# Kernel tuning notes

Measured on AMD Instinct MI355X. Metric: run time of the kernel, lower is better.

## Reference

```python
import jax, jax.numpy as jnp
import numpy as np

D = 128      # hidden_dim
NH = 4       # nhead
FF = 64      # dim_feedforward
P = 16       # patch size
C, H, W = 3, 224, 224
NA = 15      # n_actions
BS = 256
NP = (H // P) * (W // P)      # 196 patches
PD = C * P * P                # 768 patch_dim


def _ln(x, s, b):
    m = jnp.mean(x, -1, keepdims=True)
    v = jnp.mean(jnp.square(x - m), -1, keepdims=True)
    return (x - m) / jnp.sqrt(v + 1e-5) * s + b


def _mha(q, k, v, Wqkv, bqkv, Wo, bo):
    # q,k,v: (L, B, D); Wqkv: (D, 3D) jax-layout; torch MultiheadAttention math
    Wq, Wk, Wv = jnp.split(Wqkv, 3, axis=1)
    bq, bk, bv = jnp.split(bqkv, 3)
    hd = D // NH
    Lq, B, _ = q.shape
    Lk = k.shape[0]
    Q = (q @ Wq + bq).reshape(Lq, B, NH, hd)
    K = (k @ Wk + bk).reshape(Lk, B, NH, hd)
    V = (v @ Wv + bv).reshape(Lk, B, NH, hd)
    scores = jnp.einsum('qbhd,kbhd->bhqk', Q, K) * np.float32(1.0 / np.sqrt(hd))
    attn = jax.nn.softmax(scores, axis=-1)
    out = jnp.einsum('bhqk,kbhd->qbhd', attn, V).reshape(Lq, B, D)
    return out @ Wo + bo


def setup_inputs() -> dict:
    key = jax.random.key(0)
    ks = iter(jax.random.split(key, 64))
    n = lambda shape, sc=0.02: (jax.random.normal(next(ks), shape, jnp.float32) * sc)
    inp = {
        'image': jax.random.normal(next(ks), (BS, C, H, W), jnp.float32),
        'angle': jax.random.normal(next(ks), (BS,), jnp.float32),
        'pos_x': jax.random.normal(next(ks), (BS,), jnp.float32),
        'pos_y': jax.random.normal(next(ks), (BS,), jnp.float32),
        'sk': jax.random.normal(next(ks), (BS, 200), jnp.float32),
        'patch_W': n((PD, D)), 'patch_b': n((D,)),
        'pos_emb': n((NP, 1, D), 1.0),
        'enc_qkv_W': n((D, 3 * D)), 'enc_qkv_b': n((3 * D,)),
        'enc_out_W': n((D, D)), 'enc_out_b': n((D,)),
        'enc_ln1_s': jnp.ones((D,)), 'enc_ln1_b': jnp.zeros((D,)),
        'enc_ff1_W': n((D, FF)), 'enc_ff1_b': n((FF,)),
        'enc_ff2_W': n((FF, D)), 'enc_ff2_b': n((D,)),
        'enc_ln2_s': jnp.ones((D,)), 'enc_ln2_b': jnp.zeros((D,)),
        'dec_sa_qkv_W': n((D, 3 * D)), 'dec_sa_qkv_b': n((3 * D,)),
        'dec_sa_out_W': n((D, D)), 'dec_sa_out_b': n((D,)),
        'dec_ca_qkv_W': n((D, 3 * D)), 'dec_ca_qkv_b': n((3 * D,)),
        'dec_ca_out_W': n((D, D)), 'dec_ca_out_b': n((D,)),
        'dec_ln1_s': jnp.ones((D,)), 'dec_ln1_b': jnp.zeros((D,)),
        'dec_ln2_s': jnp.ones((D,)), 'dec_ln2_b': jnp.zeros((D,)),
        'dec_ln3_s': jnp.ones((D,)), 'dec_ln3_b': jnp.zeros((D,)),
        'dec_ff1_W': n((D, FF)), 'dec_ff1_b': n((FF,)),
        'dec_ff2_W': n((FF, D)), 'dec_ff2_b': n((D,)),
        'dec_norm_s': jnp.ones((D,)), 'dec_norm_b': jnp.zeros((D,)),
        'sk1_W': n((200, 256)), 'sk1_b': n((256,)),
        'sk2_W': n((256, 256)), 'sk2_b': n((256,)),
        'sk3_W': n((256, 100)), 'sk3_b': n((100,)),
        'act_W': n((NA + 103, D)), 'act_b': n((D,)),
        'l1_W': n((D, D)), 'l1_b': n((D,)),
        'l2_W': n((D, 1)), 'l2_b': n((1,)),
    }
    return inp


def reference(image, angle, pos_x, pos_y, sk,
              patch_W, patch_b, pos_emb,
              enc_qkv_W, enc_qkv_b, enc_out_W, enc_out_b,
              enc_ln1_s, enc_ln1_b, enc_ff1_W, enc_ff1_b, enc_ff2_W, enc_ff2_b,
              enc_ln2_s, enc_ln2_b,
              dec_sa_qkv_W, dec_sa_qkv_b, dec_sa_out_W, dec_sa_out_b,
              dec_ca_qkv_W, dec_ca_qkv_b, dec_ca_out_W, dec_ca_out_b,
              dec_ln1_s, dec_ln1_b, dec_ln2_s, dec_ln2_b, dec_ln3_s, dec_ln3_b,
              dec_ff1_W, dec_ff1_b, dec_ff2_W, dec_ff2_b,
              dec_norm_s, dec_norm_b,
              sk1_W, sk1_b, sk2_W, sk2_b, sk3_W, sk3_b,
              act_W, act_b, l1_W, l1_b, l2_W, l2_b):
    b = image.shape[0]
    hh, ww = H // P, W // P
    # rearrange 'b c (h p1) (w p2) -> b (h w) (p1 p2 c)'
    x = image.reshape(b, C, hh, P, ww, P).transpose(0, 2, 4, 3, 5, 1).reshape(b, hh * ww, PD)
    src = (x @ patch_W + patch_b).transpose(1, 0, 2) + pos_emb  # (n, b, D)
    # encoder layer (post-norm, dropout=eval)
    s2 = _mha(src, src, src, enc_qkv_W, enc_qkv_b, enc_out_W, enc_out_b)
    src = _ln(src + s2, enc_ln1_s, enc_ln1_b)
    ff = jax.nn.relu(src @ enc_ff1_W + enc_ff1_b) @ enc_ff2_W + enc_ff2_b
    memory = _ln(src + ff, enc_ln2_s, enc_ln2_b)
    # sketch MLP
    s = jax.nn.relu(sk @ sk1_W + sk1_b)
    s = jax.nn.relu(s @ sk2_W + sk2_b)
    s = s @ sk3_W + sk3_b  # (b, 100)
    pos_ang = jnp.stack([angle, pos_x, pos_y], axis=1)  # (b, 3)
    # batched action encoding (replaces python double loop)
    nA = NA
    eye = jnp.broadcast_to(jnp.eye(nA, dtype=image.dtype)[None], (b, nA, nA))
    feats = jnp.concatenate([
        eye,
        jnp.broadcast_to(pos_ang[:, None, :], (b, nA, 3)),
        jnp.broadcast_to(s[:, None, :], (b, nA, 100)),
    ], axis=-1)  # (b, nA, nA+103)
    tgt = (feats @ act_W + act_b).transpose(1, 0, 2)  # (nA, b, D)
    # decoder layer (post-norm)
    t2 = _mha(tgt, tgt, tgt, dec_sa_qkv_W, dec_sa_qkv_b, dec_sa_out_W, dec_sa_out_b)
    tgt = _ln(tgt + t2, dec_ln1_s, dec_ln1_b)
    t2 = _mha(tgt, memory, memory, dec_ca_qkv_W, dec_ca_qkv_b, dec_ca_out_W, dec_ca_out_b)
    tgt = _ln(tgt + t2, dec_ln2_s, dec_ln2_b)
    ff = jax.nn.relu(tgt @ dec_ff1_W + dec_ff1_b) @ dec_ff2_W + dec_ff2_b
    tgt = _ln(tgt + ff, dec_ln3_s, dec_ln3_b)
    out = _ln(tgt, dec_norm_s, dec_norm_b)  # (nA, b, D)
    out = out.transpose(1, 0, 2)  # (b, nA, D)
    q = jax.nn.relu(out @ l1_W + l1_b) @ l2_W + l2_b  # (b, nA, 1)
    return q[..., 0]  # (b, nA)
```

## Files before the change

### kernel.cpp

```cpp
#include <hip/hip_runtime.h>
#include <math.h>

#define BSZ 256
#define DIM 128
#define NHD 4
#define NPATCH 196
#define NACT 15

typedef float f32x4 __attribute__((ext_vector_type(4)));
typedef __bf16 bf16x8 __attribute__((ext_vector_type(8)));
typedef short short8 __attribute__((ext_vector_type(8)));

__device__ __forceinline__ float wred_sum(float v) {
#pragma unroll
    for (int m = 1; m < 64; m <<= 1) v += __shfl_xor(v, m, 64);
    return v;
}
__device__ __forceinline__ float wred_max(float v) {
#pragma unroll
    for (int m = 1; m < 64; m <<= 1) v = fmaxf(v, __shfl_xor(v, m, 64));
    return v;
}
__device__ __forceinline__ ushort f2bf(float f) {
    unsigned u = __float_as_uint(f);
    return (ushort)((u + 0x7fffu + ((u >> 16) & 1u)) >> 16);
}

__global__ __launch_bounds__(256) void k_wconv(
    const float* __restrict__ pW, const float* __restrict__ qkvW,
    const float* __restrict__ outW, const float* __restrict__ ff1W,
    const float* __restrict__ ff2W, const float* __restrict__ ckvW,
    ushort* __restrict__ o)
{
    int i = blockIdx.x * 256 + threadIdx.x;
    if (i < 98304) {
        int n = i / 768, kp = i % 768;
        int c = kp >> 8, q = kp & 255;
        o[i] = f2bf(pW[(q * 3 + c) * 128 + n]); return;
    }
    i -= 98304;
    if (i < 49152) { int n = i >> 7, k = i & 127; o[98304 + i] = f2bf(qkvW[k * 384 + n]); return; }
    i -= 49152;
    if (i < 16384) { int n = i >> 7, k = i & 127; o[147456 + i] = f2bf(outW[k * 128 + n]); return; }
    i -= 16384;
    if (i < 8192)  { int n = i >> 7, k = i & 127; o[163840 + i] = f2bf(ff1W[k * 64 + n]); return; }
    i -= 8192;
    if (i < 8192)  { int n = i >> 6, k = i & 63;  o[172032 + i] = f2bf(ff2W[k * 128 + n]); return; }
    i -= 8192;
    if (i < 32768) { int n = i >> 7, k = i & 127; o[180224 + i] = f2bf(ckvW[k * 384 + 128 + n]); return; }
}

__global__ __launch_bounds__(512) void k_pg_dec1(
    const float* __restrict__ img, const ushort* __restrict__ Wt,
    const float* __restrict__ pbias, const float* __restrict__ pe,
    float* __restrict__ C, ushort* __restrict__ Cb,
    const float* __restrict__ sk,
    const float* __restrict__ W1, const float* __restrict__ b1,
    const float* __restrict__ W2, const float* __restrict__ b2,
    const float* __restrict__ W3, const float* __restrict__ b3,
    const float* __restrict__ ang, const float* __restrict__ px,
    const float* __restrict__ py,
    const float* __restrict__ actW, const float* __restrict__ actb,
    const float* __restrict__ saW, const float* __restrict__ sab,
    const float* __restrict__ saoW, const float* __restrict__ saob,
    const float* __restrict__ ln1s, const float* __restrict__ ln1b,
    const float* __restrict__ caW, const float* __restrict__ cab,
    float* __restrict__ TGo, float* __restrict__ DQ)
{
    extern __shared__ char smem[];
    const int t = threadIdx.x;
    const int w = t >> 6, l = t & 63;

    if (blockIdx.x >= 256) {
        ushort* As = (ushort*)smem;
        ushort* Ws = As + 2 * 64 * 64;
        const bool act = t < 256;
        const int pb = blockIdx.x - 256;
        const int p = pb >> 2, bq = pb & 3;
        const int hp_ = p / 14, wp = p % 14;
        const int r0 = p * 256 + bq * 64;
        const int wm = w >> 1, wn = w & 1;
        const int lrow = l & 15, lk = l >> 4;
        const int arow = (t & 255) >> 2;
        const int b_img = bq * 64 + arow;
        const float* gimg = img + (size_t)b_img * 150528 + hp_ * 3584 + wp * 16;

        f32x4 acc[2][4];
#pragma unroll
        for (int m = 0; m < 2; ++m)
#pragma unroll
            for (int n = 0; n < 4; ++n) acc[m][n] = (f32x4)0.f;

        float4 va[4];
        short8 wr[4];

        auto loadT = [&](int kc) {
            if (!act) return;
            const int c = kc >> 8, p1q = (kc >> 6) & 3;
            const float* gc = gimg + c * 50176 + p1q * 896;
#pragma unroll
            for (int i = 0; i < 4; ++i)
                va[i] = *(const float4*)(gc + i * 224 + (t & 3) * 4);
#pragma unroll
            for (int j = 0; j < 4; ++j) {
                const int i2 = t + 256 * j;
                const int row = i2 >> 3, ch = i2 & 7;
                wr[j] = *(const short8*)(Wt + (size_t)row * 768 + kc + ch * 8);
            }
        };
        auto storeT = [&](int buf) {
            if (!act) return;
            ushort* Ab = As + buf * 64 * 64;
            ushort* Wb = Ws + buf * 128 * 64;
#pragma unroll
            for (int i = 0; i < 4; ++i) {
                ushort4 o4;
                o4.x = f2bf(va[i].x); o4.y = f2bf(va[i].y);
                o4.z = f2bf(va[i].z); o4.w = f2bf(va[i].w);
                const int kq = (t & 3) + 4 * i;
                const int bo = (kq * 8) ^ ((arow & 7) << 4);
                *(ushort4*)((char*)Ab + arow * 128 + bo) = o4;
            }
#pragma unroll
            for (int j = 0; j < 4; ++j) {
                const int i2 = t + 256 * j;
                const int row = i2 >> 3, ch = i2 & 7;
                const int sw = (ch * 16) ^ ((row & 7) << 4);
                *(short8*)((char*)Wb + row * 128 + sw) = wr[j];
            }
        };
        auto mfmaT = [&](int buf) {
            if (!act) return;
            const ushort* Ab = As + buf * 64 * 64;
            const ushort* Wb = Ws + buf * 128 * 64;
#pragma unroll
            for (int ks = 0; ks < 2; ++ks) {
                bf16x8 af[2], bfr[4];
#pragma unroll
                for (int m = 0; m < 2; ++m) {
                    const int row = wm * 32 + m * 16 + lrow;
                    const int col = (ks * 64 + lk * 16) ^ ((row & 7) << 4);
                    af[m] = *(const bf16x8*)((const char*)Ab + row * 128 + col);
                }
#pragma unroll
                for (int n = 0; n < 4; ++n) {
                    const int row = wn * 64 + n * 16 + lrow;
                    const int col = (ks * 64 + lk * 16) ^ ((row & 7) << 4);
                    bfr[n] = *(const bf16x8*)((const char*)Wb + row * 128 + col);
                }
#pragma unroll
                for (int m = 0; m < 2; ++m)
#pragma unroll
                    for (int n = 0; n < 4; ++n)
                        acc[m][n] = __builtin_amdgcn_mfma_f32_16x16x32_bf16(
                            af[m], bfr[n], acc[m][n], 0, 0, 0);
            }
        };

        loadT(0);
        for (int it = 0; it < 12; it += 2) {
            storeT(0);
            if (it + 1 < 12) loadT((it + 1) * 64);
            __syncthreads();
            mfmaT(0);
            storeT(1);
            if (it + 2 < 12) loadT((it + 2) * 64);
            __syncthreads();
            mfmaT(1);
        }

        if (act) {
            const int crow0 = (l >> 4) * 4;
            const int ccol = l & 15;
#pragma unroll
            for (int m = 0; m < 2; ++m) {
                const int growb = r0 + wm * 32 + m * 16 + crow0;
#pragma unroll
                for (int n = 0; n < 4; ++n) {
                    const int gcol = wn * 64 + n * 16 + ccol;
                    const float bv = pbias[gcol] + pe[p * 128 + gcol];
#pragma unroll
                    for (int j = 0; j < 4; ++j) {
                        const int grow = growb + j;
                        const float v = acc[m][n][j] + bv;
                        C[(size_t)grow * 128 + gcol] = v;
                        Cb[(size_t)grow * 128 + gcol] = f2bf(v);
                    }
                }
            }
        }
        return;
    }

    float* tg  = (float*)smem;
    float* qkv = tg + 1920;
    float* ao  = qkv + 5820;
    float* xr  = ao + 1920;
    float* h1  = xr + 256;
    float* h2  = h1 + 256;
    float* s3  = h2 + 256;
    float* pbv = s3 + 100;
    float* hp  = pbv + 64;
    const int b = blockIdx.x;

    if (t < 256) xr[t] = (t < 200) ? sk[(size_t)b * 200 + t] : 0.f;
    __syncthreads();
    {
        const int c = t & 255, g = t >> 8;
        const int k0 = g * 100;
        float a = 0.f;
#pragma unroll 10
        for (int k = k0; k < k0 + 100; ++k) a += xr[k] * W1[k * 256 + c];
        hp[g * 256 + c] = a;
    }
    __syncthreads();
    if (t < 256) h1[t] = fmaxf(hp[t] + hp[256 + t] + b1[t], 0.f);
    __syncthreads();
    {
        const int c = t & 255, g = t >> 8;
        const int k0 = g * 128;
        float a = 0.f;
#pragma unroll 8
        for (int k = k0; k < k0 + 128; ++k) a += h1[k] * W2[k * 256 + c];
        hp[g * 256 + c] = a;
    }
    __syncthreads();
    if (t < 256) h2[t] = fmaxf(hp[t] + hp[256 + t] + b2[t], 0.f);
    __syncthreads();
    if (t < 400) {
        const int c = t % 100, g = t / 100;
        const int k0 = g * 64;
        float a = 0.f;
#pragma unroll 8
        for (int k = k0; k < k0 + 64; ++k) a += h2[k] * W3[k * 100 + c];
        hp[g * 256 + c] = a;
    }
    __syncthreads();
    if (t < 100) s3[t] = hp[t] + hp[256 + t] + hp[512 + t] + hp[768 + t] + b3[t];
    __syncthreads();
    {
        const int c = t & 127, g = t >> 7;
        const int k0 = g * 25;
        float a = 0.f;
#pragma unroll 5
        for (int k = k0; k < k0 + 25; ++k) a += s3[k] * actW[(18 + k) * 128 + c];
        hp[g * 256 + c] = a;
    }
    __syncthreads();
    if (t < 128) {
        const float base = actb[t] + hp[t] + hp[256 + t] + hp[512 + t] + hp[768 + t] +
                           ang[b] * actW[15 * 128 + t] + px[b] * actW[16 * 128 + t] +
                           py[b] * actW[17 * 128 + t];
#pragma unroll
        for (int i = 0; i < 15; ++i) tg[i * 128 + t] = base + actW[i * 128 + t];
    }
    __syncthreads();

    if (t < 384) {
        float acc[15];
#pragma unroll
        for (int r = 0; r < 15; ++r) acc[r] = 0.f;
#pragma unroll 4
        for (int k = 0; k < 128; ++k) {
            const float wv = saW[(size_t)k * 384 + t];
#pragma unroll
            for (int r = 0; r < 15; ++r) acc[r] += tg[r * 128 + k] * wv;
        }
        const float bb = sab[t];
#pragma unroll
        for (int r = 0; r < 15; ++r) qkv[r * 388 + t] = acc[r] + bb;
    }
    __syncthreads();

    const float rs = 0.17677669529663687f;
    if (w < 4) {
        for (int qi = 0; qi < 15; ++qi) {
            float s = -3.0e38f;
            if (l < 15) {
                s = 0.f;
#pragma unroll
                for (int d = 0; d < 32; ++d)
                    s += qkv[qi * 388 + w * 32 + d] * qkv[l * 388 + 128 + w * 32 + d];
                s *= rs;
            }
            const float m = wred_max(s);
            const float pv = (l < 15) ? __expf(s - m) : 0.f;
            const float sum = wred_sum(pv);
            if (l < 15) pbv[w * 16 + l] = pv;
            if (l < 32) {
                float o = 0.f;
#pragma unroll
                for (int j = 0; j < 15; ++j) o += pbv[w * 16 + j] * qkv[j * 388 + 256 + w * 32 + l];
                ao[qi * 128 + w * 32 + l] = o / sum;
            }
        }
    }
    __syncthreads();

    {
        const int c = t & 127, g = t >> 7;
        const int r3 = (g + 12 < 15) ? g + 12 : 0;
        float a0 = 0.f, a1 = 0.f, a2 = 0.f, a3 = 0.f;
#pragma unroll 4
        for (int k = 0; k < 128; ++k) {
            const float wv = saoW[(size_t)k * 128 + c];
            a0 += ao[g * 128 + k] * wv;
            a1 += ao[(g + 4) * 128 + k] * wv;
            a2 += ao[(g + 8) * 128 + k] * wv;
            a3 += ao[r3 * 128 + k] * wv;
        }
        const float bb = saob[c];
        qkv[g * 388 + c]       = a0 + bb + tg[g * 128 + c];
        qkv[(g + 4) * 388 + c] = a1 + bb + tg[(g + 4) * 128 + c];
        qkv[(g + 8) * 388 + c] = a2 + bb + tg[(g + 8) * 128 + c];
        if (g + 12 < 15) qkv[(g + 12) * 388 + c] = a3 + bb + tg[(g + 12) * 128 + c];
    }
    __syncthreads();
    for (int r = w; r < 15; r += 8) {
        const float x0 = qkv[r * 388 + l], x1 = qkv[r * 388 + l + 64];
        const float sm = wred_sum(x0 + x1);
        const float sq = wred_sum(x0 * x0 + x1 * x1);
        const float mean = sm * 0.0078125f;
        const float rstd = rsqrtf(sq * 0.0078125f - mean * mean + 1e-5f);
        const float y0 = (x0 - mean) * rstd * ln1s[l] + ln1b[l];
        const float y1 = (x1 - mean) * rstd * ln1s[l + 64] + ln1b[l + 64];
        tg[r * 128 + l] = y0; tg[r * 128 + l + 64] = y1;
        float* g2 = TGo + ((size_t)r * 256 + b) * 128;
        g2[l] = y0; g2[l + 64] = y1;
    }
    __syncthreads();

    {
        const int c = t & 127, g = t >> 7;
        const int r3 = (g + 12 < 15) ? g + 12 : 0;
        float a0 = 0.f, a1 = 0.f, a2 = 0.f, a3 = 0.f;
#pragma unroll 4
        for (int k = 0; k < 128; ++k) {
            const float wv = caW[(size_t)k * 384 + c];
            a0 += tg[g * 128 + k] * wv;
            a1 += tg[(g + 4) * 128 + k] * wv;
            a2 += tg[(g + 8) * 128 + k] * wv;
            a3 += tg[r3 * 128 + k] * wv;
        }
        const float bb = cab[c];
        DQ[((size_t)g * 256 + b) * 128 + c]       = a0 + bb;
        DQ[((size_t)(g + 4) * 256 + b) * 128 + c] = a1 + bb;
        DQ[((size_t)(g + 8) * 256 + b) * 128 + c] = a2 + bb;
        if (g + 12 < 15) DQ[((size_t)(g + 12) * 256 + b) * 128 + c] = a3 + bb;
    }
}

template <int BM, int BN>
__global__ __launch_bounds__(256) void k_gemm_bf16(
    const ushort* __restrict__ A, int lda,
    const ushort* __restrict__ Wt, int K,
    const float* __restrict__ bias,
    float* __restrict__ C, ushort* __restrict__ Cb, int ldc,
    const float* __restrict__ pe, int relu)
{
    constexpr int NWN = BN / 64;
    constexpr int NWM = 4 / NWN;
    constexpr int WTM = BM / NWM;
    constexpr int MF = WTM / 16;
    __shared__ ushort As[BM * 64];
    __shared__ ushort Ws[BN * 64];
    const int t = threadIdx.x;
    const int w = t >> 6, l = t & 63;
    const int r0 = blockIdx.x * BM;
    const int n0 = blockIdx.y * BN;
    const int wm = w / NWN, wn = w % NWN;
    const int lrow = l & 15, lk = l >> 4;

    f32x4 acc[MF][4];
#pragma unroll
    for (int m = 0; m < MF; ++m)
#pragma unroll
        for (int n = 0; n < 4; ++n) acc[m][n] = (f32x4)0.f;

    for (int kc = 0; kc < K; kc += 64) {
        __syncthreads();
#pragma unroll
        for (int i = t; i < BM * 8; i += 256) {
            const int row = i >> 3, ch = i & 7;
            const int sw = (ch * 16) ^ ((row & 7) << 4);
            *(short8*)((char*)As + row * 128 + sw) =
                *(const short8*)(A + (size_t)(r0 + row) * lda + kc + ch * 8);
        }
#pragma unroll
        for (int i = t; i < BN * 8; i += 256) {
            const int row = i >> 3, ch = i & 7;
            const int sw = (ch * 16) ^ ((row & 7) << 4);
            *(short8*)((char*)Ws + row * 128 + sw) =
                *(const short8*)(Wt + (size_t)(n0 + row) * K + kc + ch * 8);
        }
        __syncthreads();
#pragma unroll
        for (int ks = 0; ks < 2; ++ks) {
            bf16x8 af[MF], bfr[4];
#pragma unroll
            for (int m = 0; m < MF; ++m) {
                const int row = wm * WTM + m * 16 + lrow;
                const int col = (ks * 64 + lk * 16) ^ ((row & 7) << 4);
                af[m] = *(const bf16x8*)((const char*)As + row * 128 + col);
            }
#pragma unroll
            for (int n = 0; n < 4; ++n) {
                const int row = wn * 64 + n * 16 + lrow;
                const int col = (ks * 64 + lk * 16) ^ ((row & 7) << 4);
                bfr[n] = *(const bf16x8*)((const char*)Ws + row * 128 + col);
            }
#pragma unroll
            for (int m = 0; m < MF; ++m)
#pragma unroll
                for (int n = 0; n < 4; ++n)
                    acc[m][n] = __builtin_amdgcn_mfma_f32_16x16x32_bf16(
                        af[m], bfr[n], acc[m][n], 0, 0, 0);
        }
    }

    const int crow0 = (l >> 4) * 4;
    const int ccol = l & 15;
#pragma unroll
    for (int m = 0; m < MF; ++m) {
        const int growb = r0 + wm * WTM + m * 16 + crow0;
#pragma unroll
        for (int n = 0; n < 4; ++n) {
            const int gcol = n0 + wn * 64 + n * 16 + ccol;
            const float bv = bias[gcol];
#pragma unroll
            for (int j = 0; j < 4; ++j) {
                const int grow = growb + j;
                float v = acc[m][n][j] + bv;
                if (pe) v += pe[(grow >> 8) * 128 + gcol];
                if (relu) v = fmaxf(v, 0.f);
                if (C)  C[(size_t)grow * ldc + gcol] = v;
                if (Cb) Cb[(size_t)grow * ldc + gcol] = f2bf(v);
            }
        }
    }
}

__global__ __launch_bounds__(256) void k_gemm_ln(
    const ushort* __restrict__ A, int lda,
    const ushort* __restrict__ Wt, int K,
    const float* __restrict__ bias,
    const float* __restrict__ resid,
    const float* __restrict__ lns, const float* __restrict__ lnbi,
    float* __restrict__ Co, ushort* __restrict__ Cb)
{
    __shared__ ushort As[64 * 64];
    __shared__ ushort Ws[128 * 64];
    __shared__ float psum[64][2][2];
    const int t = threadIdx.x;
    const int w = t >> 6, l = t & 63;
    const int r0 = blockIdx.x * 64;
    const int wm = w >> 1, wn = w & 1;
    const int lrow = l & 15, lk = l >> 4;

    f32x4 acc[2][4];
#pragma unroll
    for (int m = 0; m < 2; ++m)
#pragma unroll
        for (int n = 0; n < 4; ++n) acc[m][n] = (f32x4)0.f;

    for (int kc = 0; kc < K; kc += 64) {
        __syncthreads();
#pragma unroll
        for (int i = t; i < 64 * 8; i += 256) {
            const int row = i >> 3, ch = i & 7;
            const int sw = (ch * 16) ^ ((row & 7) << 4);
            *(short8*)((char*)As + row * 128 + sw) =
                *(const short8*)(A + (size_t)(r0 + row) * lda + kc + ch * 8);
        }
#pragma unroll
        for (int i = t; i < 128 * 8; i += 256) {
            const int row = i >> 3, ch = i & 7;
            const int sw = (ch * 16) ^ ((row & 7) << 4);
            *(short8*)((char*)Ws + row * 128 + sw) =
                *(const short8*)(Wt + (size_t)row * K + kc + ch * 8);
        }
        __syncthreads();
#pragma unroll
        for (int ks = 0; ks < 2; ++ks) {
            bf16x8 af[2], bfr[4];
#pragma unroll
            for (int m = 0; m < 2; ++m) {
                const int row = wm * 32 + m * 16 + lrow;
                const int col = (ks * 64 + lk * 16) ^ ((row & 7) << 4);
                af[m] = *(const bf16x8*)((const char*)As + row * 128 + col);
            }
#pragma unroll
            for (int n = 0; n < 4; ++n) {
                const int row = wn * 64 + n * 16 + lrow;
                const int col = (ks * 64 + lk * 16) ^ ((row & 7) << 4);
                bfr[n] = *(const bf16x8*)((const char*)Ws + row * 128 + col);
            }
#pragma unroll
            for (int m = 0; m < 2; ++m)
#pragma unroll
                for (int n = 0; n < 4; ++n)
                    acc[m][n] = __builtin_amdgcn_mfma_f32_16x16x32_bf16(
                        af[m], bfr[n], acc[m][n], 0, 0, 0);
        }
    }

    const int crow0 = (l >> 4) * 4;
    const int ccol = l & 15;
#pragma unroll
    for (int m = 0; m < 2; ++m) {
        const int growb = r0 + wm * 32 + m * 16 + crow0;
#pragma unroll
        for (int n = 0; n < 4; ++n) {
            const int gcol = wn * 64 + n * 16 + ccol;
            const float bv = bias[gcol];
#pragma unroll
            for (int j = 0; j < 4; ++j) {
                float v = acc[m][n][j] + bv;
                if (resid) v += resid[(size_t)(growb + j) * 128 + gcol];
                acc[m][n][j] = v;
            }
        }
    }
#pragma unroll
    for (int m = 0; m < 2; ++m)
#pragma unroll
        for (int j = 0; j < 4; ++j) {
            float s_ = 0.f, q_ = 0.f;
#pragma unroll
            for (int n = 0; n < 4; ++n) {
                const float x = acc[m][n][j];
                s_ += x; q_ += x * x;
            }
#pragma unroll
            for (int mk = 1; mk < 16; mk <<= 1) {
                s_ += __shfl_xor(s_, mk, 64);
                q_ += __shfl_xor(q_, mk, 64);
            }
            if (ccol == 0) {
                const int r = wm * 32 + m * 16 + crow0 + j;
                psum[r][wn][0] = s_;
                psum[r][wn][1] = q_;
            }
        }
    __syncthreads();
    float mean_[2][4], rstd_[2][4];
#pragma unroll
    for (int m = 0; m < 2; ++m)
#pragma unroll
        for (int j = 0; j < 4; ++j) {
            const int r = wm * 32 + m * 16 + crow0 + j;
            const float sum = psum[r][0][0] + psum[r][1][0];
            const float sq  = psum[r][0][1] + psum[r][1][1];
            const float mean = sum * 0.0078125f;
            const float var = sq * 0.0078125f - mean * mean;
            mean_[m][j] = mean;
            rstd_[m][j] = rsqrtf(var + 1e-5f);
        }
#pragma unroll
    for (int m = 0; m < 2; ++m) {
        const int growb = r0 + wm * 32 + m * 16 + crow0;
#pragma unroll
        for (int n = 0; n < 4; ++n) {
            const int gcol = wn * 64 + n * 16 + ccol;
            const float sv = lns[gcol], bv2 = lnbi[gcol];
#pragma unroll
            for (int j = 0; j < 4; ++j) {
                const float y = (acc[m][n][j] - mean_[m][j]) * rstd_[m][j] * sv + bv2;
                const size_t oi = (size_t)(growb + j) * 128 + gcol;
                if (Co) Co[oi] = y;
                if (Cb) Cb[oi] = f2bf(y);
            }
        }
    }
}

__global__ __launch_bounds__(256) void k_attn_mfma(
    const ushort* __restrict__ qkv, ushort* __restrict__ ob, float scale)
{
    __shared__ ushort Ks[208 * 40];
    __shared__ ushort Vt[32 * 232];
    __shared__ ushort Ps[4][16 * 232];
    const int bh = blockIdx.x;
    const int b = bh >> 2, h = bh & 3;
    const int t = threadIdx.x, w = t >> 6, l = t & 63;
    const int lr = l & 15, lg = l >> 4;

    for (int idx = t; idx < 784; idx += 256) {
        const int j = idx >> 2, ch = idx & 3;
        const size_t base = ((size_t)j * 256 + b) * 384 + h * 32 + ch * 8;
        *(short8*)(Ks + j * 40 + ch * 8) = *(const short8*)(qkv + base + 128);
        short8 v = *(const short8*)(qkv + base + 256);
#pragma unroll
        for (int q = 0; q < 8; ++q)
            Vt[(ch * 8 + q) * 232 + j] = (ushort)v[q];
    }
    for (int idx = t; idx < 32 * 36; idx += 256)
        Vt[(idx / 36) * 232 + 196 + (idx % 36)] = 0;
    for (int i = l; i < 256; i += 64)
        Ps[w][(i >> 4) * 232 + 208 + (i & 15)] = 0;
    __syncthreads();

    for (int qt = w; qt < 13; qt += 4) {
        int qr = qt * 16 + lr; if (qr > 195) qr = 195;
        const bf16x8 qf = *(const bf16x8*)(qkv + ((size_t)qr * 256 + b) * 384 + h * 32 + lg * 8);

        f32x4 s[13];
#pragma unroll
        for (int jn = 0; jn < 13; ++jn) {
            const bf16x8 kf = *(const bf16x8*)(Ks + (jn * 16 + lr) * 40 + lg * 8);
            s[jn] = __builtin_amdgcn_mfma_f32_16x16x32_bf16(qf, kf, (f32x4)0.f, 0, 0, 0);
        }
        if (lr >= 4) {
            s[12][0] = -3.0e38f; s[12][1] = -3.0e38f;
            s[12][2] = -3.0e38f; s[12][3] = -3.0e38f;
        }

        float inv[4];
        ushort* pw = Ps[w];
#pragma unroll
        for (int j = 0; j < 4; ++j) {
            float m = s[0][j];
#pragma unroll
            for (int jn = 1; jn < 13; ++jn) m = fmaxf(m, s[jn][j]);
            m = fmaxf(m, __shfl_xor(m, 1, 64));
            m = fmaxf(m, __shfl_xor(m, 2, 64));
            m = fmaxf(m, __shfl_xor(m, 4, 64));
            m = fmaxf(m, __shfl_xor(m, 8, 64));
            float sum = 0.f;
#pragma unroll
            for (int jn = 0; jn < 13; ++jn) {
                const float p = __expf((s[jn][j] - m) * scale);
                s[jn][j] = p;
                sum += p;
            }
            sum += __shfl_xor(sum, 1, 64);
            sum += __shfl_xor(sum, 2, 64);
            sum += __shfl_xor(sum, 4, 64);
            sum += __shfl_xor(sum, 8, 64);
            inv[j] = 1.0f / sum;
        }
#pragma unroll
        for (int jn = 0; jn < 13; ++jn)
#pragma unroll
            for (int j = 0; j < 4; ++j)
                pw[(lg * 4 + j) * 232 + jn * 16 + lr] = f2bf(s[jn][j]);

        f32x4 o0 = (f32x4)0.f, o1 = (f32x4)0.f;
#pragma unroll
        for (int kt = 0; kt < 7; ++kt) {
            const bf16x8 pf = *(const bf16x8*)(pw + lr * 232 + kt * 32 + lg * 8);
            const bf16x8 v0 = *(const bf16x8*)(Vt + lr * 232 + kt * 32 + lg * 8);
            const bf16x8 v1 = *(const bf16x8*)(Vt + (16 + lr) * 232 + kt * 32 + lg * 8);
            o0 = __builtin_amdgcn_mfma_f32_16x16x32_bf16(pf, v0, o0, 0, 0, 0);
            o1 = __builtin_amdgcn_mfma_f32_16x16x32_bf16(pf, v1, o1, 0, 0, 0);
        }
#pragma unroll
        for (int j = 0; j < 4; ++j) {
            const int r = qt * 16 + lg * 4 + j;
            if (r < 196) {
                const size_t o = ((size_t)r * 256 + b) * 128 + h * 32;
                ob[o + lr]      = f2bf(o0[j] * inv[j]);
                ob[o + 16 + lr] = f2bf(o1[j] * inv[j]);
            }
        }
    }
}

__global__ __launch_bounds__(256) void k_attn(
    const float* __restrict__ qp, int qstride,
    const float* __restrict__ kvp, int kvstride, int koff, int voff,
    float* __restrict__ op, ushort* __restrict__ ob,
    int Lq, int Lk, float scale)
{
    __shared__ float Kl[196 * 36];
    __shared__ float Vl[196 * 32];
    __shared__ float pbuf[4][256];
    const int bh = blockIdx.x;
    const int b = bh >> 2;
    const int h = bh & 3;
    const int t = threadIdx.x;
    const int w = t >> 6;
    const int l = t & 63;

    for (int idx = t; idx < Lk * 8; idx += 256) {
        const int j = idx >> 3;
        const int kq = idx & 7;
        const size_t row = ((size_t)j * 256 + b) * kvstride + h * 32 + kq * 4;
        *(float4*)(&Kl[j * 36 + kq * 4]) = *(const float4*)(kvp + row + koff);
        *(float4*)(&Vl[j * 32 + kq * 4]) = *(const float4*)(kvp + row + voff);
    }
    if ((Lk & 1) && t < 8) *(float4*)(&Vl[Lk * 32 + t * 4]) = make_float4(0.f, 0.f, 0.f, 0.f);
    __syncthreads();

    const int Lh = (Lk + 1) >> 1;
    const int half = l >> 5;
    const int kk = l & 31;
    const int jb = half * Lh;

    for (int jq = w; jq < Lq; jq += 4) {
        const float* qrow = qp + ((size_t)jq * 256 + b) * qstride + h * 32;
        float4 q4[8];
#pragma unroll
        for (int kq = 0; kq < 8; ++kq) q4[kq] = *(const float4*)(qrow + kq * 4);

        float s[4];
#pragma unroll
        for (int r = 0; r < 4; ++r) {
            const int j = l + (r << 6);
            float acc = -3.0e38f;
            if (j < Lk) {
                acc = 0.f;
#pragma unroll
                for (int kq = 0; kq < 8; ++kq) {
                    const float4 kv = *(const float4*)(&Kl[j * 36 + kq * 4]);
                    acc += q4[kq].x * kv.x + q4[kq].y * kv.y +
                           q4[kq].z * kv.z + q4[kq].w * kv.w;
                }
                acc *= scale;
            }
            s[r] = acc;
        }
        float m = fmaxf(fmaxf(s[0], s[1]), fmaxf(s[2], s[3]));
        m = wred_max(m);
        float sum = 0.f;
#pragma unroll
        for (int r = 0; r < 4; ++r) {
            const int j = l + (r << 6);
            float p = __expf(s[r] - m);
            if (j >= Lk) p = 0.f;
            pbuf[w][j] = p;
            sum += p;
        }
        sum = wred_sum(sum);
        const float inv = 1.0f / sum;
        __threadfence_block();

        float o = 0.f;
        for (int jj = 0; jj < Lh; ++jj) {
            const float pv = pbuf[w][jb + jj];
            const float vv = Vl[(jb + jj) * 32 + kk];
            o += pv * vv;
        }
        o += __shfl_xor(o, 32, 64);
        o *= inv;
        if (l < 32) {
            const size_t oi = ((size_t)jq * 256 + b) * 128 + h * 32 + l;
            if (op) op[oi] = o;
            if (ob) ob[oi] = f2bf(o);
        }
        __threadfence_block();
    }
}

__global__ __launch_bounds__(512) void k_dec2(
    const float* __restrict__ TGo, const float* __restrict__ AT,
    const float* __restrict__ caoW, const float* __restrict__ caob,
    const float* __restrict__ ln2s, const float* __restrict__ ln2b,
    const float* __restrict__ ff1W, const float* __restrict__ ff1b,
    const float* __restrict__ ff2W, const float* __restrict__ ff2b,
    const float* __restrict__ ln3s, const float* __restrict__ ln3b,
    const float* __restrict__ ns, const float* __restrict__ nb,
    const float* __restrict__ l1W, const float* __restrict__ l1b,
    const float* __restrict__ l2w, const float* __restrict__ l2b,
    float* __restrict__ qout)
{
    __shared__ float tg[15][128], ao[15][128], o2[15][128];
    __shared__ float ff[15][64];
    const int b = blockIdx.x, t = threadIdx.x;
    const int w = t >> 6, l = t & 63;

    for (int idx = t; idx < 1920; idx += 512) {
        const int r = idx >> 7, c = idx & 127;
        tg[r][c] = TGo[((size_t)r * 256 + b) * 128 + c];
        ao[r][c] = AT[((size_t)r * 256 + b) * 128 + c];
    }
    __syncthreads();

    {
        const int c = t & 127, g = t >> 7;
        const int r3 = (g + 12 < 15) ? g + 12 : 0;
        float a0 = 0.f, a1 = 0.f, a2 = 0.f, a3 = 0.f;
#pragma unroll 4
        for (int k = 0; k < 128; ++k) {
            const float wv = caoW[(size_t)k * 128 + c];
            a0 += ao[g][k] * wv;
            a1 += ao[g + 4][k] * wv;
            a2 += ao[g + 8][k] * wv;
            a3 += ao[r3][k] * wv;
        }
        const float bb = caob[c];
        o2[g][c]     = a0 + bb + tg[g][c];
        o2[g + 4][c] = a1 + bb + tg[g + 4][c];
        o2[g + 8][c] = a2 + bb + tg[g + 8][c];
        if (g + 12 < 15) o2[g + 12][c] = a3 + bb + tg[g + 12][c];
    }
    __syncthreads();
    for (int r = w; r < 15; r += 8) {
        const float x0 = o2[r][l], x1 = o2[r][l + 64];
        const float sm = wred_sum(x0 + x1);
        const float sq = wred_sum(x0 * x0 + x1 * x1);
        const float mean = sm * 0.0078125f;
        const float rstd = rsqrtf(sq * 0.0078125f - mean * mean + 1e-5f);
        tg[r][l]      = (x0 - mean) * rstd * ln2s[l] + ln2b[l];
        tg[r][l + 64] = (x1 - mean) * rstd * ln2s[l + 64] + ln2b[l + 64];
    }
    __syncthreads();
    {
        const int n = t & 63, g = t >> 6;
        const int r1 = (g + 8 < 15) ? g + 8 : 0;
        float a0 = 0.f, a1 = 0.f;
#pragma unroll 4
        for (int k = 0; k < 128; ++k) {
            const float wv = ff1W[(size_t)k * 64 + n];
            a0 += tg[g][k] * wv;
            a1 += tg[r1][k] * wv;
        }
        const float bb = ff1b[n];
        ff[g][n] = fmaxf(a0 + bb, 0.f);
        if (g + 8 < 15) ff[g + 8][n] = fmaxf(a1 + bb, 0.f);
    }
    __syncthreads();
    {
        const int c = t & 127, g = t >> 7;
        const int r3 = (g + 12 < 15) ? g + 12 : 0;
        float a0 = 0.f, a1 = 0.f, a2 = 0.f, a3 = 0.f;
#pragma unroll 4
        for (int k = 0; k < 64; ++k) {
            const float wv = ff2W[(size_t)k * 128 + c];
            a0 += ff[g][k] * wv;
            a1 += ff[g + 4][k] * wv;
            a2 += ff[g + 8][k] * wv;
            a3 += ff[r3][k] * wv;
        }
        const float bb = ff2b[c];
        o2[g][c]     = a0 + bb + tg[g][c];
        o2[g + 4][c] = a1 + bb + tg[g + 4][c];
        o2[g + 8][c] = a2 + bb + tg[g + 8][c];
        if (g + 12 < 15) o2[g + 12][c] = a3 + bb + tg[g + 12][c];
    }
    __syncthreads();
    for (int r = w; r < 15; r += 8) {
        const float x0 = o2[r][l], x1 = o2[r][l + 64];
        const float sm = wred_sum(x0 + x1);
        const float sq = wred_sum(x0 * x0 + x1 * x1);
        const float mean = sm * 0.0078125f;
        const float rstd = rsqrtf(sq * 0.0078125f - mean * mean + 1e-5f);
        const float y0 = (x0 - mean) * rstd * ln3s[l] + ln3b[l];
        const float y1 = (x1 - mean) * rstd * ln3s[l + 64] + ln3b[l + 64];
        const float sm2 = wred_sum(y0 + y1);
        const float sq2 = wred_sum(y0 * y0 + y1 * y1);
        const float mean2 = sm2 * 0.0078125f;
        const float rstd2 = rsqrtf(sq2 * 0.0078125f - mean2 * mean2 + 1e-5f);
        tg[r][l]      = (y0 - mean2) * rstd2 * ns[l] + nb[l];
        tg[r][l + 64] = (y1 - mean2) * rstd2 * ns[l + 64] + nb[l + 64];
    }
    __syncthreads();
    {
        const int c = t & 127, g = t >> 7;
        const int r3 = (g + 12 < 15) ? g + 12 : 0;
        float a0 = 0.f, a1 = 0.f, a2 = 0.f, a3 = 0.f;
#pragma unroll 4
        for (int k = 0; k < 128; ++k) {
            const float wv = l1W[(size_t)k * 128 + c];
            a0 += tg[g][k] * wv;
            a1 += tg[g + 4][k] * wv;
            a2 += tg[g + 8][k] * wv;
            a3 += tg[r3][k] * wv;
        }
        const float bb = l1b[c];
        o2[g][c]     = fmaxf(a0 + bb, 0.f);
        o2[g + 4][c] = fmaxf(a1 + bb, 0.f);
        o2[g + 8][c] = fmaxf(a2 + bb, 0.f);
        if (g + 12 < 15) o2[g + 12][c] = fmaxf(a3 + bb, 0.f);
    }
    __syncthreads();
    for (int r = w; r < 15; r += 8) {
        const float d = wred_sum(o2[r][l] * l2w[l] + o2[r][l + 64] * l2w[l + 64]);
        if (l == 0) qout[b * 15 + r] = d + l2b[0];
    }
}

extern "C" void kernel_launch(void* const* d_in, const int* in_sizes, int n_in,
                              void* d_out, int out_size, void* d_ws, size_t ws_size,
                              hipStream_t stream)
{
    (void)in_sizes; (void)n_in; (void)out_size; (void)ws_size;
    const float* image      = (const float*)d_in[0];
    const float* angle      = (const float*)d_in[1];
    const float* pos_x      = (const float*)d_in[2];
    const float* pos_y      = (const float*)d_in[3];
    const float* sk         = (const float*)d_in[4];
    const float* patch_W    = (const float*)d_in[5];
    const float* patch_b    = (const float*)d_in[6];
    const float* pos_emb    = (const float*)d_in[7];
    const float* enc_qkv_W  = (const float*)d_in[8];
    const float* enc_qkv_b  = (const float*)d_in[9];
    const float* enc_out_W  = (const float*)d_in[10];
    const float* enc_out_b  = (const float*)d_in[11];
    const float* enc_ln1_s  = (const float*)d_in[12];
    const float* enc_ln1_b  = (const float*)d_in[13];
    const float* enc_ff1_W  = (const float*)d_in[14];
    const float* enc_ff1_b  = (const float*)d_in[15];
    const float* enc_ff2_W  = (const float*)d_in[16];
    const float* enc_ff2_b  = (const float*)d_in[17];
    const float* enc_ln2_s  = (const float*)d_in[18];
    const float* enc_ln2_b  = (const float*)d_in[19];
    const float* dec_sa_qkv_W = (const float*)d_in[20];
    const float* dec_sa_qkv_b = (const float*)d_in[21];
    const float* dec_sa_out_W = (const float*)d_in[22];
    const float* dec_sa_out_b = (const float*)d_in[23];
    const float* dec_ca_qkv_W = (const float*)d_in[24];
    const float* dec_ca_qkv_b = (const float*)d_in[25];
    const float* dec_ca_out_W = (const float*)d_in[26];
    const float* dec_ca_out_b = (const float*)d_in[27];
    const float* dec_ln1_s  = (const float*)d_in[28];
    const float* dec_ln1_b  = (const float*)d_in[29];
    const float* dec_ln2_s  = (const float*)d_in[30];
    const float* dec_ln2_b  = (const float*)d_in[31];
    const float* dec_ln3_s  = (const float*)d_in[32];
    const float* dec_ln3_b  = (const float*)d_in[33];
    const float* dec_ff1_W  = (const float*)d_in[34];
    const float* dec_ff1_b  = (const float*)d_in[35];
    const float* dec_ff2_W  = (const float*)d_in[36];
    const float* dec_ff2_b  = (const float*)d_in[37];
    const float* dec_norm_s = (const float*)d_in[38];
    const float* dec_norm_b = (const float*)d_in[39];
    const float* sk1_W = (const float*)d_in[40];
    const float* sk1_b = (const float*)d_in[41];
    const float* sk2_W = (const float*)d_in[42];
    const float* sk2_b = (const float*)d_in[43];
    const float* sk3_W = (const float*)d_in[44];
    const float* sk3_b = (const float*)d_in[45];
    const float* act_W = (const float*)d_in[46];
    const float* act_b = (const float*)d_in[47];
    const float* l1_W  = (const float*)d_in[48];
    const float* l1_b  = (const float*)d_in[49];
    const float* l2_W  = (const float*)d_in[50];
    const float* l2_b  = (const float*)d_in[51];

    float* ws = (float*)d_ws;
    float* S0   = ws;
    float* QKVr = ws + 6422528;
    float* T0   = ws + 25690112;
    float* T1   = ws + 32112640;
    float* F1   = ws + 38535168;
    float* M0r  = ws + 41746432;
    float* S1s  = ws + 48168960;
    float* TG   = S1s + 156672;
    ushort* WTS = (ushort*)(ws + 48817152);

    ushort* QKVb = (ushort*)QKVr;
    float*  KV   = QKVr;
    float* DQ   = QKVr + 14319616;
    float* DT0  = T0;
    ushort* srcb = (ushort*)M0r;
    ushort* T0b  = (ushort*)M0r;
    ushort* lnb  = (ushort*)(M0r + 3211264);
    ushort* F1b  = (ushort*)F1;
    ushort* M0b  = (ushort*)T1;
    ushort* wt_patch = WTS;
    ushort* wt_qkv   = WTS + 98304;
    ushort* wt_out   = WTS + 147456;
    ushort* wt_ff1   = WTS + 163840;
    ushort* wt_ff2   = WTS + 172032;
    ushort* wt_ckv   = WTS + 180224;

    const float rs = 0.17677669529663687f;

    k_wconv<<<dim3(832), 256, 0, stream>>>(patch_W, enc_qkv_W, enc_out_W,
                                           enc_ff1_W, enc_ff2_W, dec_ca_qkv_W, WTS);

    k_pg_dec1<<<dim3(1040), 512, 49152, stream>>>(
        image, wt_patch, patch_b, pos_emb, S0, srcb,
        sk, sk1_W, sk1_b, sk2_W, sk2_b, sk3_W, sk3_b,
        angle, pos_x, pos_y, act_W, act_b,
        dec_sa_qkv_W, dec_sa_qkv_b, dec_sa_out_W, dec_sa_out_b,
        dec_ln1_s, dec_ln1_b, dec_ca_qkv_W, dec_ca_qkv_b, TG, DQ);

    k_gemm_bf16<64, 128><<<dim3(784, 3), 256, 0, stream>>>(
        srcb, 128, wt_qkv, 128, enc_qkv_b, nullptr, QKVb, 384, nullptr, 0);
    k_attn_mfma<<<dim3(1024), 256, 0, stream>>>(QKVb, T0b, rs);
    k_gemm_ln<<<dim3(784), 256, 0, stream>>>(
        T0b, 128, wt_out, 128, enc_out_b, S0, enc_ln1_s, enc_ln1_b, S0, lnb);
    k_gemm_bf16<64, 64><<<dim3(784, 1), 256, 0, stream>>>(
        lnb, 128, wt_ff1, 128, enc_ff1_b, nullptr, F1b, 64, nullptr, 1);
    k_gemm_ln<<<dim3(784), 256, 0, stream>>>(
        F1b, 64, wt_ff2, 64, enc_ff2_b, S0, enc_ln2_s, enc_ln2_b, nullptr, M0b);
    k_gemm_bf16<64, 128><<<dim3(784, 2), 256, 0, stream>>>(
        M0b, 128, wt_ckv, 128, dec_ca_qkv_b + 128, KV, nullptr, 256, nullptr, 0);

    k_attn<<<dim3(1024), 256, 0, stream>>>(DQ, 128, KV, 256, 0, 128,
                                           DT0, nullptr, 15, 196, rs);
    k_dec2<<<dim3(256), 512, 0, stream>>>(
        TG, DT0, dec_ca_out_W, dec_ca_out_b, dec_ln2_s, dec_ln2_b,
        dec_ff1_W, dec_ff1_b, dec_ff2_W, dec_ff2_b,
        dec_ln3_s, dec_ln3_b, dec_norm_s, dec_norm_b,
        l1_W, l1_b, l2_W, l2_b, (float*)d_out);
}
```

Baseline: 344.9 us.

## Fuse encoder FF1 GEMM into out-proj LayerNorm kernel and enlarge QKV GEMM tiles

The out-projection+LN1 kernel now also runs the FF1 GEMM with ReLU on its normalized tile. It stages the LN output as bf16 in shared memory and the FF1 weights in a new shared buffer, which removes a separate launch and the round trip of the bf16 LN output through global memory. The encoder QKV and cross-attention KV GEMMs also switch from 64-row to 128-row tiles, halving the grid. The fused kernel uses more shared memory, and the larger tiles mean fewer blocks, which could lower occupancy.

```diff
diff --git a/kernel.cpp b/kernel.cpp
--- a/kernel.cpp
+++ b/kernel.cpp
@@ -440,17 +440,21 @@
     }
 }
 
+template <int FF>
 __global__ __launch_bounds__(256) void k_gemm_ln(
     const ushort* __restrict__ A, int lda,
     const ushort* __restrict__ Wt, int K,
     const float* __restrict__ bias,
     const float* __restrict__ resid,
     const float* __restrict__ lns, const float* __restrict__ lnbi,
-    float* __restrict__ Co, ushort* __restrict__ Cb)
+    float* __restrict__ Co, ushort* __restrict__ Cb,
+    const ushort* __restrict__ ffW, const float* __restrict__ ffb,
+    ushort* __restrict__ Fb)
 {
     __shared__ ushort As[64 * 64];
     __shared__ ushort Ws[128 * 64];
     __shared__ float psum[64][2][2];
+    __shared__ ushort ffWs[FF ? 64 * 128 : 2];
     const int t = threadIdx.x;
     const int w = t >> 6, l = t & 63;
     const int r0 = blockIdx.x * 64;
@@ -566,9 +570,60 @@
 #pragma unroll
             for (int j = 0; j < 4; ++j) {
                 const float y = (acc[m][n][j] - mean_[m][j]) * rstd_[m][j] * sv + bv2;
+                acc[m][n][j] = y;
                 const size_t oi = (size_t)(growb + j) * 128 + gcol;
                 if (Co) Co[oi] = y;
                 if (Cb) Cb[oi] = f2bf(y);
+            }
+        }
+    }
+
+    if constexpr (FF) {
+#pragma unroll
+        for (int m = 0; m < 2; ++m) {
+            const int rowb = wm * 32 + m * 16 + crow0;
+#pragma unroll
+            for (int n = 0; n < 4; ++n) {
+                const int c = wn * 64 + n * 16 + ccol;
+                const int cb = ((c >> 3) * 16) ^ 0;
+#pragma unroll
+                for (int j = 0; j < 4; ++j) {
+                    const int row = rowb + j;
+                    const int bo = row * 256 + ((cb) ^ ((row & 7) << 4)) + (c & 7) * 2;
+                    *(ushort*)((char*)Ws + bo) = f2bf(acc[m][n][j]);
+                }
+            }
+        }
+        for (int i = t; i < 1024; i += 256) {
+            const int row = i >> 4, ch = i & 15;
+            *(short8*)((char*)ffWs + row * 256 + ((ch * 16) ^ ((row & 7) << 4))) =
+                *(const short8*)(ffW + (size_t)row * 128 + ch * 8);
+        }
+        __syncthreads();
+        f32x4 accF[4];
+#pragma unroll
+        for (int n = 0; n < 4; ++n) accF[n] = (f32x4)0.f;
+#pragma unroll
+        for (int ks = 0; ks < 4; ++ks) {
+            const int arow2 = w * 16 + lrow;
+            const int acol = (ks * 64 + lk * 16) ^ ((arow2 & 7) << 4);
+            const bf16x8 af = *(const bf16x8*)((const char*)Ws + arow2 * 256 + acol);
+#pragma unroll
+            for (int n = 0; n < 4; ++n) {
+                const int brow = n * 16 + lrow;
+                const int bcol = (ks * 64 + lk * 16) ^ ((brow & 7) << 4);
+                const bf16x8 bf = *(const bf16x8*)((const char*)ffWs + brow * 256 + bcol);
+                accF[n] = __builtin_amdgcn_mfma_f32_16x16x32_bf16(af, bf, accF[n], 0, 0, 0);
+            }
+        }
+#pragma unroll
+        for (int n = 0; n < 4; ++n) {
+            const int gcol = n * 16 + ccol;
+            const float bb = ffb[gcol];
+#pragma unroll
+            for (int j = 0; j < 4; ++j) {
+                const int grow = r0 + w * 16 + crow0 + j;
+                Fb[(size_t)grow * 64 + gcol] = f2bf(fmaxf(accF[n][j] + bb, 0.f));
             }
         }
     }
@@ -955,7 +1010,6 @@
     float* DT0  = T0;
     ushort* srcb = (ushort*)M0r;
     ushort* T0b  = (ushort*)M0r;
-    ushort* lnb  = (ushort*)(M0r + 3211264);
     ushort* F1b  = (ushort*)F1;
     ushort* M0b  = (ushort*)T1;
     ushort* wt_patch = WTS;
@@ -977,16 +1031,16 @@
         dec_sa_qkv_W, dec_sa_qkv_b, dec_sa_out_W, dec_sa_out_b,
         dec_ln1_s, dec_ln1_b, dec_ca_qkv_W, dec_ca_qkv_b, TG, DQ);
 
-    k_gemm_bf16<64, 128><<<dim3(784, 3), 256, 0, stream>>>(
+    k_gemm_bf16<128, 128><<<dim3(392, 3), 256, 0, stream>>>(
         srcb, 128, wt_qkv, 128, enc_qkv_b, nullptr, QKVb, 384, nullptr, 0);
     k_attn_mfma<<<dim3(1024), 256, 0, stream>>>(QKVb, T0b, rs);
-    k_gemm_ln<<<dim3(784), 256, 0, stream>>>(
-        T0b, 128, wt_out, 128, enc_out_b, S0, enc_ln1_s, enc_ln1_b, S0, lnb);
-    k_gemm_bf16<64, 64><<<dim3(784, 1), 256, 0, stream>>>(
-        lnb, 128, wt_ff1, 128, enc_ff1_b, nullptr, F1b, 64, nullptr, 1);
-    k_gemm_ln<<<dim3(784), 256, 0, stream>>>(
-        F1b, 64, wt_ff2, 64, enc_ff2_b, S0, enc_ln2_s, enc_ln2_b, nullptr, M0b);
-    k_gemm_bf16<64, 128><<<dim3(784, 2), 256, 0, stream>>>(
+    k_gemm_ln<1><<<dim3(784), 256, 0, stream>>>(
+        T0b, 128, wt_out, 128, enc_out_b, S0, enc_ln1_s, enc_ln1_b, S0, nullptr,
+        wt_ff1, enc_ff1_b, F1b);
+    k_gemm_ln<0><<<dim3(784), 256, 0, stream>>>(
+        F1b, 64, wt_ff2, 64, enc_ff2_b, S0, enc_ln2_s, enc_ln2_b, nullptr, M0b,
+        nullptr, nullptr, nullptr);
+    k_gemm_bf16<128, 128><<<dim3(392, 2), 256, 0, stream>>>(
         M0b, 128, wt_ckv, 128, dec_ca_qkv_b + 128, KV, nullptr, 256, nullptr, 0);
 
     k_attn<<<dim3(1024), 256, 0, stream>>>(DQ, 128, KV, 256, 0, 128,
```

Result: faster. 315.0 us (median of 2 runs) (-8.7%).
